# Performance work log

Hardware: AMD Instinct MI355X
Metric: run time of the kernel (lower is better)

## Reference

```python
import jax, jax.numpy as jnp
import numpy as np

CLIP_LIMIT = 10.0
NTILES = 8        # OpenCV createCLAHE default tileGridSize=(8,8)
NBINS = 256

_M_RGB2XYZ = jnp.array([[0.412453, 0.357580, 0.180423],
                        [0.212671, 0.715160, 0.072169],
                        [0.019334, 0.119193, 0.950227]], dtype=jnp.float32)
_M_XYZ2RGB = jnp.array([[ 3.240479, -1.537150, -0.498535],
                        [-0.969256,  1.875992,  0.041556],
                        [ 0.055648, -0.204043,  1.057311]], dtype=jnp.float32)
_WP = jnp.array([0.950456, 1.0, 1.088754], dtype=jnp.float32)  # D65 white point (OpenCV)
_EPS = 0.008856


def rgb2lab(rgb):  # rgb: [H,W,3] in [0,1]
    xyz = jnp.einsum('hwc,dc->hwd', rgb, _M_RGB2XYZ) / _WP
    f = jnp.where(xyz > _EPS, jnp.cbrt(xyz), 7.787 * xyz + 16.0 / 116.0)
    fx, fy, fz = f[..., 0], f[..., 1], f[..., 2]
    L = 116.0 * fy - 16.0
    a = 500.0 * (fx - fy)
    b = 200.0 * (fy - fz)
    return L, a, b


def lab2rgb(L, a, b):
    fy = (L + 16.0) / 116.0
    fx = fy + a / 500.0
    fz = fy - b / 200.0
    f = jnp.stack([fx, fy, fz], axis=-1)
    xyz = jnp.where(f ** 3 > _EPS, f ** 3, (f - 16.0 / 116.0) / 7.787) * _WP
    rgb = jnp.einsum('hwd,cd->hwc', xyz, _M_XYZ2RGB)
    return jnp.clip(rgb, 0.0, 1.0)


def clahe_channel(L8, clip_limit):
    # L8: [H,W] int32 in [0,255]
    H, W = L8.shape
    th, tw = H // NTILES, W // NTILES
    area = float(th * tw)
    # per-tile histograms via one scatter-add
    rows = jnp.arange(H) // th            # [H] tile row id
    cols = jnp.arange(W) // tw            # [W] tile col id
    tid = rows[:, None] * NTILES + cols[None, :]          # [H,W]
    flat = (tid * NBINS + L8).ravel()
    hist = jnp.zeros(NTILES * NTILES * NBINS, jnp.float32).at[flat].add(1.0)
    hist = hist.reshape(NTILES * NTILES, NBINS)
    # clip + uniform redistribution of excess
    clip = max(clip_limit * area / NBINS, 1.0)
    excess = jnp.sum(jnp.maximum(hist - clip, 0.0), axis=1, keepdims=True)
    hist = jnp.minimum(hist, clip) + excess / NBINS
    # CDF -> LUT (OpenCV: lutScale = 255/tileArea, rounded)
    cdf = jnp.cumsum(hist, axis=1)
    lut = jnp.clip(jnp.round(cdf * (255.0 / area)), 0.0, 255.0)  # [T, 256]
    # bilinear interpolation between tile LUTs
    fy = jnp.clip((jnp.arange(H, dtype=jnp.float32) + 0.5) / th - 0.5, 0.0, NTILES - 1.0)
    fx = jnp.clip((jnp.arange(W, dtype=jnp.float32) + 0.5) / tw - 0.5, 0.0, NTILES - 1.0)
    y0 = jnp.floor(fy).astype(jnp.int32); y1 = jnp.minimum(y0 + 1, NTILES - 1)
    x0 = jnp.floor(fx).astype(jnp.int32); x1 = jnp.minimum(x0 + 1, NTILES - 1)
    wy = (fy - y0)[:, None]; wx = (fx - x0)[None, :]
    def g(yi, xi):  # gather LUT value for each pixel from tile (yi, xi)
        return lut[yi[:, None] * NTILES + xi[None, :], L8]
    top = (1.0 - wx) * g(y0, x0) + wx * g(y0, x1)
    bot = (1.0 - wx) * g(y1, x0) + wx * g(y1, x1)
    return (1.0 - wy) * top + wy * bot   # [H,W] float in [0,255]


def setup_inputs() -> dict:
    key = jax.random.key(0)
    x = jax.random.uniform(key, (3, 2048, 2048), dtype=jnp.float32)
    return {"x": x}


def reference(x) -> jnp.ndarray:
    hwc = jnp.transpose(x, (1, 2, 0))          # CHW -> HWC
    L, a, b = rgb2lab(hwc)                      # L in [0,100]
    L8 = jnp.clip(jnp.round(L * (255.0 / 100.0)), 0, 255).astype(jnp.int32)
    L_eq = clahe_channel(L8, CLIP_LIMIT) * (100.0 / 255.0)
    rgb = lab2rgb(L_eq, a, b)
    return jnp.transpose(rgb, (2, 0, 1))        # HWC -> CHW
```

## Files before the change

kernel.cpp:

```cpp
#include <hip/hip_runtime.h>
#include <stdint.h>

#define HW 4194304
#define WIDTH 2048
#define NBLK 2048
#define F(x) ((float)(x))

__device__ __forceinline__ float cbrtf_glibc(float x) {
    unsigned int bits = __float_as_uint(x);
    int xe = (int)((bits >> 23) & 0xFF) - 126;
    float xm = __uint_as_float((bits & 0x007FFFFFu) | 0x3F000000u);

    double xmd = (double)xm;
    double p = __dsub_rn(0.697570460207922770, __dmul_rn(0.191502161678719066, xmd));
    p = __dadd_rn(0.492659620528969547, __dmul_rn(p, xmd));
    float u = (float)p;

    float t2 = __fmul_rn(__fmul_rn(u, u), u);

    double ud  = (double)u;
    double t2d = (double)t2;
    double num = __dmul_rn(ud, __dadd_rn(t2d, __dmul_rn(2.0, xmd)));
    double den = __dadd_rn(__dmul_rn(2.0, t2d), xmd);

    int idx = 2 + (xe % 3);
    double f = (idx == 2) ? 1.0
             : (idx == 0) ? (1.0 / 1.5874010519681994748)
             : (idx == 1) ? (1.0 / 1.2599210498948731648)
             : (idx == 3) ? 1.2599210498948731648
             :              1.5874010519681994748;
    double ym  = __dmul_rn(__ddiv_rn(num, den), f);
    float ymf = (float)ym;

    int q = xe / 3;
    float s = (q == 0) ? 1.0f : ((q == -1) ? 0.5f : 0.25f);
    return __fmul_rn(ymf, s);
}

__device__ __forceinline__ void rgb2lab_px(float r, float g, float b,
                                           int& l8, float& A_, float& B_) {
    float X = __fadd_rn(__fadd_rn(__fmul_rn(r, F(0.412453)), __fmul_rn(g, F(0.357580))), __fmul_rn(b, F(0.180423)));
    float Y = __fadd_rn(__fadd_rn(__fmul_rn(r, F(0.212671)), __fmul_rn(g, F(0.715160))), __fmul_rn(b, F(0.072169)));
    float Z = __fadd_rn(__fadd_rn(__fmul_rn(r, F(0.019334)), __fmul_rn(g, F(0.119193))), __fmul_rn(b, F(0.950227)));
    X = __fdiv_rn(X, F(0.950456));
    Z = __fdiv_rn(Z, F(1.088754));
    const float EPS = F(0.008856);
    const float C0  = F(16.0 / 116.0);
    float fx = (X > EPS) ? cbrtf_glibc(X) : __fadd_rn(__fmul_rn(F(7.787), X), C0);
    float fy = (Y > EPS) ? cbrtf_glibc(Y) : __fadd_rn(__fmul_rn(F(7.787), Y), C0);
    float fz = (Z > EPS) ? cbrtf_glibc(Z) : __fadd_rn(__fmul_rn(F(7.787), Z), C0);
    float L  = __fsub_rn(__fmul_rn(F(116.0), fy), F(16.0));
    A_ = __fmul_rn(F(500.0), __fsub_rn(fx, fy));
    B_ = __fmul_rn(F(200.0), __fsub_rn(fy, fz));
    float Lr = rintf(__fmul_rn(L, F(255.0 / 100.0)));
    Lr = fminf(fmaxf(Lr, 0.0f), 255.0f);
    l8 = (int)Lr;
}

__device__ __forceinline__ void lab2rgb_px(float Leq, float A_, float B_,
                                           float& rr, float& gg, float& bb) {
    const float EPS = F(0.008856);
    const float C0  = F(16.0 / 116.0);
    float fy2 = __fdiv_rn(__fadd_rn(Leq, 16.0f), 116.0f);
    float fx2 = __fadd_rn(fy2, __fdiv_rn(A_, 500.0f));
    float fz2 = __fsub_rn(fy2, __fdiv_rn(B_, 200.0f));
    float t3;
    t3 = fx2 * fx2 * fx2;
    float X = ((t3 > EPS) ? t3 : __fdiv_rn(__fsub_rn(fx2, C0), F(7.787))) * F(0.950456);
    t3 = fy2 * fy2 * fy2;
    float Y = ((t3 > EPS) ? t3 : __fdiv_rn(__fsub_rn(fy2, C0), F(7.787))) * F(1.0);
    t3 = fz2 * fz2 * fz2;
    float Z = ((t3 > EPS) ? t3 : __fdiv_rn(__fsub_rn(fz2, C0), F(7.787))) * F(1.088754);
    rr = __fadd_rn(__fadd_rn(__fmul_rn(X, F(3.240479)),  __fmul_rn(Y, F(-1.537150))), __fmul_rn(Z, F(-0.498535)));
    gg = __fadd_rn(__fadd_rn(__fmul_rn(X, F(-0.969256)), __fmul_rn(Y, F(1.875992))),  __fmul_rn(Z, F(0.041556)));
    bb = __fadd_rn(__fadd_rn(__fmul_rn(X, F(0.055648)),  __fmul_rn(Y, F(-0.204043))), __fmul_rn(Z, F(1.057311)));
    rr = fminf(fmaxf(rr, 0.0f), 1.0f);
    gg = fminf(fmaxf(gg, 0.0f), 1.0f);
    bb = fminf(fmaxf(bb, 0.0f), 1.0f);
}

template<bool ATOMIC_LOADS>
__device__ __forceinline__ void build_luts(const unsigned int* __restrict__ hist,
                                           float* lutS, int y0, int y1, int t) {
    const int lane = t & 63;
    const int w = t >> 6;
    #pragma unroll
    for (int i = 0; i < 4; ++i) {
        int gidx = w * 4 + i;
        int trow = gidx >> 3;
        int tcol = gidx & 7;
        int tile = (trow ? y1 : y0) * 8 + tcol;
        float h0, h1, h2, h3;
        if (ATOMIC_LOADS) {
            const unsigned int* hp = hist + tile * 256 + lane * 4;
            h0 = (float)__hip_atomic_load(&hp[0], __ATOMIC_RELAXED, __HIP_MEMORY_SCOPE_AGENT);
            h1 = (float)__hip_atomic_load(&hp[1], __ATOMIC_RELAXED, __HIP_MEMORY_SCOPE_AGENT);
            h2 = (float)__hip_atomic_load(&hp[2], __ATOMIC_RELAXED, __HIP_MEMORY_SCOPE_AGENT);
            h3 = (float)__hip_atomic_load(&hp[3], __ATOMIC_RELAXED, __HIP_MEMORY_SCOPE_AGENT);
        } else {
            uint4 hv = *(const uint4*)(hist + tile * 256 + lane * 4);
            h0 = (float)hv.x; h1 = (float)hv.y; h2 = (float)hv.z; h3 = (float)hv.w;
        }
        float e = __fadd_rn(__fadd_rn(fmaxf(h0 - 2560.0f, 0.0f),
                                      fmaxf(h1 - 2560.0f, 0.0f)),
                            __fadd_rn(fmaxf(h2 - 2560.0f, 0.0f),
                                      fmaxf(h3 - 2560.0f, 0.0f)));
        #pragma unroll
        for (int d = 1; d < 64; d <<= 1) e = __fadd_rn(e, __shfl_xor(e, d));
        float ex = __fmul_rn(e, F(1.0 / 256.0));
        float v0 = __fadd_rn(fminf(h0, 2560.0f), ex);
        float v1 = __fadd_rn(fminf(h1, 2560.0f), ex);
        float v2 = __fadd_rn(fminf(h2, 2560.0f), ex);
        float v3 = __fadd_rn(fminf(h3, 2560.0f), ex);
        float s0 = v0;
        float s1 = __fadd_rn(s0, v1);
        float s2 = __fadd_rn(s1, v2);
        float s3 = __fadd_rn(s2, v3);
        float sc = s3;
        #pragma unroll
        for (int d = 1; d < 64; d <<= 1) {
            float u2 = __shfl_up(sc, d);
            if (lane >= d) sc = __fadd_rn(sc, u2);
        }
        float excl = __fsub_rn(sc, s3);
        int lb = trow * 2048 + tcol * 256 + lane * 4;
        float c0 = rintf(__fmul_rn(__fadd_rn(excl, s0), F(255.0 / 65536.0)));
        float c1 = rintf(__fmul_rn(__fadd_rn(excl, s1), F(255.0 / 65536.0)));
        float c2 = rintf(__fmul_rn(__fadd_rn(excl, s2), F(255.0 / 65536.0)));
        float c3 = rintf(__fmul_rn(__fadd_rn(excl, s3), F(255.0 / 65536.0)));
        lutS[lb + 0] = fminf(fmaxf(c0, 0.0f), 255.0f);
        lutS[lb + 1] = fminf(fmaxf(c1, 0.0f), 255.0f);
        lutS[lb + 2] = fminf(fmaxf(c2, 0.0f), 255.0f);
        lutS[lb + 3] = fminf(fmaxf(c3, 0.0f), 255.0f);
    }
}

__device__ __forceinline__ void apply4(const float* lutS, int col0, int idx,
        int l80, int l81, int l82, int l83,
        float A0, float A1, float A2, float A3,
        float B0, float B1, float B2, float B3,
        float wy, float omwy, float* __restrict__ out) {
    float4 o_r, o_g, o_b;
#define PIX(J, L8V, AV, BV, OR_, OG_, OB_) {                                      \
    int col = col0 + (J);                                                         \
    float fxc = fminf(fmaxf(((float)col + 0.5f) * (1.0f / 256.0f) - 0.5f, 0.0f), 7.0f); \
    int xi0 = (int)floorf(fxc);                                                   \
    int xi1 = min(xi0 + 1, 7);                                                    \
    float wx = __fsub_rn(fxc, (float)xi0);                                        \
    float omwx = __fsub_rn(1.0f, wx);                                             \
    float g00 = lutS[xi0 * 256 + (L8V)];                                          \
    float g01 = lutS[xi1 * 256 + (L8V)];                                          \
    float g10 = lutS[2048 + xi0 * 256 + (L8V)];                                   \
    float g11 = lutS[2048 + xi1 * 256 + (L8V)];                                   \
    float top_ = __fadd_rn(__fmul_rn(omwx, g00), __fmul_rn(wx, g01));             \
    float bot_ = __fadd_rn(__fmul_rn(omwx, g10), __fmul_rn(wx, g11));             \
    float Leq = __fmul_rn(__fadd_rn(__fmul_rn(omwy, top_), __fmul_rn(wy, bot_)),  \
                          F(100.0 / 255.0));                                      \
    lab2rgb_px(Leq, (AV), (BV), (OR_), (OG_), (OB_));                             \
}
    PIX(0, l80, A0, B0, o_r.x, o_g.x, o_b.x);
    PIX(1, l81, A1, B1, o_r.y, o_g.y, o_b.y);
    PIX(2, l82, A2, B2, o_r.z, o_g.z, o_b.z);
    PIX(3, l83, A3, B3, o_r.w, o_g.w, o_b.w);
#undef PIX
    *(float4*)(out + idx)          = o_r;
    *(float4*)(out + idx + HW)     = o_g;
    *(float4*)(out + idx + 2 * HW) = o_b;
}

__global__ __launch_bounds__(256, 8) void k_fused(const float* __restrict__ x,
        unsigned int* __restrict__ hist, unsigned int* __restrict__ rowdone,
        float* __restrict__ Abuf, float* __restrict__ Bbuf,
        unsigned int* __restrict__ l8buf, float* __restrict__ out) {
    __shared__ float lutS[4096];
    unsigned int* h = (unsigned int*)lutS;
    const int t = threadIdx.x;
    const int y = blockIdx.x;

    #pragma unroll
    for (int i = 0; i < 8; ++i) h[i * 256 + t] = 0;
    __syncthreads();

    const int rowbase = y * WIDTH;
    #pragma unroll
    for (int ch = 0; ch < 2; ++ch) {
        const int col0 = ch * 1024 + 4 * t;
        const int idx  = rowbase + col0;
        float4 r4 = *(const float4*)(x + idx);
        float4 g4 = *(const float4*)(x + idx + HW);
        float4 b4 = *(const float4*)(x + idx + 2 * HW);
        int l80, l81, l82, l83;
        float A0, A1, A2, A3, B0, B1, B2, B3;
        rgb2lab_px(r4.x, g4.x, b4.x, l80, A0, B0);
        rgb2lab_px(r4.y, g4.y, b4.y, l81, A1, B1);
        rgb2lab_px(r4.z, g4.z, b4.z, l82, A2, B2);
        rgb2lab_px(r4.w, g4.w, b4.w, l83, A3, B3);
        const int hb = (col0 >> 8) << 8;
        atomicAdd(&h[hb + l80], 1u);
        atomicAdd(&h[hb + l81], 1u);
        atomicAdd(&h[hb + l82], 1u);
        atomicAdd(&h[hb + l83], 1u);
        *(float4*)(Abuf + idx) = make_float4(A0, A1, A2, A3);
        *(float4*)(Bbuf + idx) = make_float4(B0, B1, B2, B3);
        l8buf[idx >> 2] = (unsigned)l80 | ((unsigned)l81 << 8)
                        | ((unsigned)l82 << 16) | ((unsigned)l83 << 24);
    }
    __syncthreads();
    {
        unsigned int* gh = hist + (y >> 8) * 2048;
        #pragma unroll
        for (int i = 0; i < 8; ++i) {
            unsigned int v = h[i * 256 + t];
            if (v) atomicAdd(&gh[i * 256 + t], v);
        }
    }
    __syncthreads();

    float fyc = fminf(fmaxf(((float)y + 0.5f) * (1.0f / 256.0f) - 0.5f, 0.0f), 7.0f);
    int y0 = (int)floorf(fyc);
    int y1 = min(y0 + 1, 7);
    float wy = __fsub_rn(fyc, (float)y0);
    float omwy = __fsub_rn(1.0f, wy);

    if (t == 0) {
        __threadfence();
        atomicAdd(&rowdone[y >> 8], 1u);
        long limit = 1L << 18;
        while (limit-- > 0) {
            unsigned a = __hip_atomic_load(&rowdone[y0], __ATOMIC_ACQUIRE, __HIP_MEMORY_SCOPE_AGENT);
            unsigned b = __hip_atomic_load(&rowdone[y1], __ATOMIC_ACQUIRE, __HIP_MEMORY_SCOPE_AGENT);
            if (a == 256u && b == 256u) break;
            __builtin_amdgcn_s_sleep(2);
        }
    }
    __syncthreads();

    build_luts<true>(hist, lutS, y0, y1, t);
    __syncthreads();

    #pragma unroll
    for (int ch = 0; ch < 2; ++ch) {
        const int col0 = ch * 1024 + 4 * t;
        const int idx  = rowbase + col0;
        float4 a4 = *(const float4*)(Abuf + idx);
        float4 b4 = *(const float4*)(Bbuf + idx);
        unsigned p = l8buf[idx >> 2];
        apply4(lutS, col0, idx,
               (int)(p & 0xFFu), (int)((p >> 8) & 0xFFu),
               (int)((p >> 16) & 0xFFu), (int)((p >> 24) & 0xFFu),
               a4.x, a4.y, a4.z, a4.w, b4.x, b4.y, b4.z, b4.w,
               wy, omwy, out);
    }
}

__global__ __launch_bounds__(256, 8) void k_hist_ab(const float* __restrict__ x,
        unsigned int* __restrict__ hist,
        float* __restrict__ Abuf, float* __restrict__ Bbuf,
        unsigned int* __restrict__ l8buf, int store) {
    __shared__ unsigned int h[2048];
    const int t = threadIdx.x;
    const int y = blockIdx.x;
    #pragma unroll
    for (int i = 0; i < 8; ++i) h[i * 256 + t] = 0;
    __syncthreads();

    const int rowbase = y * WIDTH;
    #pragma unroll
    for (int ch = 0; ch < 2; ++ch) {
        const int col0 = ch * 1024 + 4 * t;
        const int idx  = rowbase + col0;
        float4 r4 = *(const float4*)(x + idx);
        float4 g4 = *(const float4*)(x + idx + HW);
        float4 b4 = *(const float4*)(x + idx + 2 * HW);
        int l80, l81, l82, l83;
        float A0, A1, A2, A3, B0, B1, B2, B3;
        rgb2lab_px(r4.x, g4.x, b4.x, l80, A0, B0);
        rgb2lab_px(r4.y, g4.y, b4.y, l81, A1, B1);
        rgb2lab_px(r4.z, g4.z, b4.z, l82, A2, B2);
        rgb2lab_px(r4.w, g4.w, b4.w, l83, A3, B3);
        const int hb = (col0 >> 8) << 8;
        atomicAdd(&h[hb + l80], 1u);
        atomicAdd(&h[hb + l81], 1u);
        atomicAdd(&h[hb + l82], 1u);
        atomicAdd(&h[hb + l83], 1u);
        if (store) {
            *(float4*)(Abuf + idx) = make_float4(A0, A1, A2, A3);
            *(float4*)(Bbuf + idx) = make_float4(B0, B1, B2, B3);
            l8buf[idx >> 2] = (unsigned)l80 | ((unsigned)l81 << 8)
                            | ((unsigned)l82 << 16) | ((unsigned)l83 << 24);
        }
    }
    __syncthreads();
    unsigned int* gh = hist + (y >> 8) * 2048;
    #pragma unroll
    for (int i = 0; i < 8; ++i) {
        unsigned int v = h[i * 256 + t];
        if (v) atomicAdd(&gh[i * 256 + t], v);
    }
}

__global__ __launch_bounds__(256, 8) void k_lut_apply(const float* __restrict__ x,
        const unsigned int* __restrict__ hist,
        const float* __restrict__ Abuf, const float* __restrict__ Bbuf,
        const unsigned int* __restrict__ l8buf,
        float* __restrict__ out, int stored) {
    __shared__ float lutS[4096];
    const int t = threadIdx.x;
    const int y = blockIdx.x;

    float fyc = fminf(fmaxf(((float)y + 0.5f) * (1.0f / 256.0f) - 0.5f, 0.0f), 7.0f);
    int y0 = (int)floorf(fyc);
    int y1 = min(y0 + 1, 7);
    float wy = __fsub_rn(fyc, (float)y0);
    float omwy = __fsub_rn(1.0f, wy);

    build_luts<false>(hist, lutS, y0, y1, t);
    __syncthreads();

    const int rowbase = y * WIDTH;
    #pragma unroll
    for (int ch = 0; ch < 2; ++ch) {
        const int col0 = ch * 1024 + 4 * t;
        const int idx  = rowbase + col0;
        float A0, A1, A2, A3, B0, B1, B2, B3;
        int l80, l81, l82, l83;
        if (stored) {
            float4 a4 = *(const float4*)(Abuf + idx);
            float4 b4 = *(const float4*)(Bbuf + idx);
            unsigned p = l8buf[idx >> 2];
            A0 = a4.x; A1 = a4.y; A2 = a4.z; A3 = a4.w;
            B0 = b4.x; B1 = b4.y; B2 = b4.z; B3 = b4.w;
            l80 = (int)(p & 0xFFu); l81 = (int)((p >> 8) & 0xFFu);
            l82 = (int)((p >> 16) & 0xFFu); l83 = (int)((p >> 24) & 0xFFu);
        } else {
            float4 r4 = *(const float4*)(x + idx);
            float4 g4 = *(const float4*)(x + idx + HW);
            float4 b4 = *(const float4*)(x + idx + 2 * HW);
            rgb2lab_px(r4.x, g4.x, b4.x, l80, A0, B0);
            rgb2lab_px(r4.y, g4.y, b4.y, l81, A1, B1);
            rgb2lab_px(r4.z, g4.z, b4.z, l82, A2, B2);
            rgb2lab_px(r4.w, g4.w, b4.w, l83, A3, B3);
        }
        apply4(lutS, col0, idx, l80, l81, l82, l83,
               A0, A1, A2, A3, B0, B1, B2, B3, wy, omwy, out);
    }
}

extern "C" void kernel_launch(void* const* d_in, const int* in_sizes, int n_in,
                              void* d_out, int out_size, void* d_ws, size_t ws_size,
                              hipStream_t stream) {
    const float* x = (const float*)d_in[0];
    float* out = (float*)d_out;
    char* ws = (char*)d_ws;
    unsigned int* hist = (unsigned int*)ws;
    unsigned int* rowdone = (unsigned int*)(ws + 65536);
    const size_t off = 131072;
    float* Abuf = (float*)(ws + off);
    float* Bbuf = (float*)(ws + off + (size_t)HW * 4);
    unsigned int* l8buf = (unsigned int*)(ws + off + (size_t)HW * 8);
    const size_t need = off + (size_t)HW * 9;
    const int store = (ws_size >= need) ? 1 : 0;

    static int fused_ok = -1;
    if (fused_ok < 0) {
        int nb = 0, ncu = 0, dev = 0;
        (void)hipGetDevice(&dev);
        hipError_t e1 = hipOccupancyMaxActiveBlocksPerMultiprocessor(&nb, k_fused, 256, 0);
        hipError_t e2 = hipDeviceGetAttribute(&ncu, hipDeviceAttributeMultiprocessorCount, dev);
        fused_ok = (e1 == hipSuccess && e2 == hipSuccess && nb * ncu >= NBLK) ? 1 : 0;
    }

    (void)hipMemsetAsync(ws, 0, 65536 + 64, stream);

    if (fused_ok == 1 && store == 1) {
        k_fused<<<NBLK, 256, 0, stream>>>(x, hist, rowdone, Abuf, Bbuf, l8buf, out);
    } else {
        k_hist_ab<<<NBLK, 256, 0, stream>>>(x, hist, Abuf, Bbuf, l8buf, store);
        k_lut_apply<<<NBLK, 256, 0, stream>>>(x, hist, Abuf, Bbuf, l8buf, out, store);
    }
}
```

Baseline: 128.3 us.

## Keep per-pixel Lab intermediates in registers across the grid-wide histogram barrier

Adds a fused kernel variant that holds each thread's a/b values and packed L8 bins in registers while it waits for the neighbouring tile-row histograms. This removes the global-memory round trip through the workspace A/B/L8 buffers. The host picks this variant when occupancy allows all 2048 blocks to be co-resident and the kernel has no register spills. Otherwise it falls back to the workspace-based fused kernel or the two-kernel path. Higher register pressure could lower occupancy, and that would disable the path or risk deadlock in the spin-wait if the occupancy check misleads.

```diff
diff --git a/kernel.cpp b/kernel.cpp
--- a/kernel.cpp
+++ b/kernel.cpp
@@ -168,7 +168,103 @@
     *(float4*)(out + idx + 2 * HW) = o_b;
 }
 
-__global__ __launch_bounds__(256, 8) void k_fused(const float* __restrict__ x,
+__global__ __launch_bounds__(256, 8) void k_fused_reg(const float* __restrict__ x,
+        unsigned int* __restrict__ hist, unsigned int* __restrict__ rowdone,
+        float* __restrict__ out) {
+    __shared__ float lutS[4096];
+    unsigned int* h = (unsigned int*)lutS;
+    const int t = threadIdx.x;
+    const int y = blockIdx.x;
+
+    #pragma unroll
+    for (int i = 0; i < 8; ++i) h[i * 256 + t] = 0;
+    __syncthreads();
+
+    const int rowbase = y * WIDTH;
+
+    float A0, A1, A2, A3, A4, A5, A6, A7;
+    float B0, B1, B2, B3, B4, B5, B6, B7;
+    unsigned pk0, pk1;
+    {
+        const int col0 = 4 * t;
+        const int idx  = rowbase + col0;
+        float4 r4 = *(const float4*)(x + idx);
+        float4 g4 = *(const float4*)(x + idx + HW);
+        float4 b4 = *(const float4*)(x + idx + 2 * HW);
+        int l0, l1, l2, l3;
+        rgb2lab_px(r4.x, g4.x, b4.x, l0, A0, B0);
+        rgb2lab_px(r4.y, g4.y, b4.y, l1, A1, B1);
+        rgb2lab_px(r4.z, g4.z, b4.z, l2, A2, B2);
+        rgb2lab_px(r4.w, g4.w, b4.w, l3, A3, B3);
+        const int hb = (col0 >> 8) << 8;
+        atomicAdd(&h[hb + l0], 1u);
+        atomicAdd(&h[hb + l1], 1u);
+        atomicAdd(&h[hb + l2], 1u);
+        atomicAdd(&h[hb + l3], 1u);
+        pk0 = (unsigned)l0 | ((unsigned)l1 << 8) | ((unsigned)l2 << 16) | ((unsigned)l3 << 24);
+    }
+    {
+        const int col0 = 1024 + 4 * t;
+        const int idx  = rowbase + col0;
+        float4 r4 = *(const float4*)(x + idx);
+        float4 g4 = *(const float4*)(x + idx + HW);
+        float4 b4 = *(const float4*)(x + idx + 2 * HW);
+        int l0, l1, l2, l3;
+        rgb2lab_px(r4.x, g4.x, b4.x, l0, A4, B4);
+        rgb2lab_px(r4.y, g4.y, b4.y, l1, A5, B5);
+        rgb2lab_px(r4.z, g4.z, b4.z, l2, A6, B6);
+        rgb2lab_px(r4.w, g4.w, b4.w, l3, A7, B7);
+        const int hb = (col0 >> 8) << 8;
+        atomicAdd(&h[hb + l0], 1u);
+        atomicAdd(&h[hb + l1], 1u);
+        atomicAdd(&h[hb + l2], 1u);
+        atomicAdd(&h[hb + l3], 1u);
+        pk1 = (unsigned)l0 | ((unsigned)l1 << 8) | ((unsigned)l2 << 16) | ((unsigned)l3 << 24);
+    }
+    __syncthreads();
+    {
+        unsigned int* gh = hist + (y >> 8) * 2048;
+        #pragma unroll
+        for (int i = 0; i < 8; ++i) {
+            unsigned int v = h[i * 256 + t];
+            if (v) atomicAdd(&gh[i * 256 + t], v);
+        }
+    }
+    __syncthreads();
+
+    float fyc = fminf(fmaxf(((float)y + 0.5f) * (1.0f / 256.0f) - 0.5f, 0.0f), 7.0f);
+    int y0 = (int)floorf(fyc);
+    int y1 = min(y0 + 1, 7);
+    float wy = __fsub_rn(fyc, (float)y0);
+    float omwy = __fsub_rn(1.0f, wy);
+
+    if (t == 0) {
+        __threadfence();
+        atomicAdd(&rowdone[y >> 8], 1u);
+        long limit = 1L << 18;
+        while (limit-- > 0) {
+            unsigned a = __hip_atomic_load(&rowdone[y0], __ATOMIC_ACQUIRE, __HIP_MEMORY_SCOPE_AGENT);
+            unsigned b = __hip_atomic_load(&rowdone[y1], __ATOMIC_ACQUIRE, __HIP_MEMORY_SCOPE_AGENT);
+            if (a == 256u && b == 256u) break;
+            __builtin_amdgcn_s_sleep(2);
+        }
+    }
+    __syncthreads();
+
+    build_luts<true>(hist, lutS, y0, y1, t);
+    __syncthreads();
+
+    apply4(lutS, 4 * t, rowbase + 4 * t,
+           (int)(pk0 & 0xFFu), (int)((pk0 >> 8) & 0xFFu),
+           (int)((pk0 >> 16) & 0xFFu), (int)((pk0 >> 24) & 0xFFu),
+           A0, A1, A2, A3, B0, B1, B2, B3, wy, omwy, out);
+    apply4(lutS, 1024 + 4 * t, rowbase + 1024 + 4 * t,
+           (int)(pk1 & 0xFFu), (int)((pk1 >> 8) & 0xFFu),
+           (int)((pk1 >> 16) & 0xFFu), (int)((pk1 >> 24) & 0xFFu),
+           A4, A5, A6, A7, B4, B5, B6, B7, wy, omwy, out);
+}
+
+__global__ __launch_bounds__(256, 8) void k_fused_ws(const float* __restrict__ x,
         unsigned int* __restrict__ hist, unsigned int* __restrict__ rowdone,
         float* __restrict__ Abuf, float* __restrict__ Bbuf,
         unsigned int* __restrict__ l8buf, float* __restrict__ out) {
@@ -361,19 +457,30 @@
     const size_t need = off + (size_t)HW * 9;
     const int store = (ws_size >= need) ? 1 : 0;
 
-    static int fused_ok = -1;
-    if (fused_ok < 0) {
-        int nb = 0, ncu = 0, dev = 0;
+    static int mode = -1;
+    if (mode < 0) {
+        int ncu = 0, dev = 0;
         (void)hipGetDevice(&dev);
-        hipError_t e1 = hipOccupancyMaxActiveBlocksPerMultiprocessor(&nb, k_fused, 256, 0);
-        hipError_t e2 = hipDeviceGetAttribute(&ncu, hipDeviceAttributeMultiprocessorCount, dev);
-        fused_ok = (e1 == hipSuccess && e2 == hipSuccess && nb * ncu >= NBLK) ? 1 : 0;
+        (void)hipDeviceGetAttribute(&ncu, hipDeviceAttributeMultiprocessorCount, dev);
+        int nbR = 0, nbW = 0;
+        bool occR = (hipOccupancyMaxActiveBlocksPerMultiprocessor(&nbR, k_fused_reg, 256, 0) == hipSuccess)
+                    && (nbR * ncu >= NBLK);
+        bool occW = (hipOccupancyMaxActiveBlocksPerMultiprocessor(&nbW, k_fused_ws, 256, 0) == hipSuccess)
+                    && (nbW * ncu >= NBLK);
+        hipFuncAttributes fa{};
+        bool nospill = (hipFuncGetAttributes(&fa, (const void*)k_fused_reg) == hipSuccess)
+                       && (fa.localSizeBytes == 0);
+        if (occR && nospill)            mode = 0;
+        else if (occW && store == 1)    mode = 1;
+        else                            mode = 2;
     }
 
     (void)hipMemsetAsync(ws, 0, 65536 + 64, stream);
 
-    if (fused_ok == 1 && store == 1) {
-        k_fused<<<NBLK, 256, 0, stream>>>(x, hist, rowdone, Abuf, Bbuf, l8buf, out);
+    if (mode == 0) {
+        k_fused_reg<<<NBLK, 256, 0, stream>>>(x, hist, rowdone, out);
+    } else if (mode == 1) {
+        k_fused_ws<<<NBLK, 256, 0, stream>>>(x, hist, rowdone, Abuf, Bbuf, l8buf, out);
     } else {
         k_hist_ab<<<NBLK, 256, 0, stream>>>(x, hist, Abuf, Bbuf, l8buf, store);
         k_lut_apply<<<NBLK, 256, 0, stream>>>(x, hist, Abuf, Bbuf, l8buf, out, store);
```

Result: no change. 128.3 us (-0.0%).
